# Kernel optimization log

Hardware: AMD Instinct MI355X
Metric: run time of the kernel (lower is better)

The kernel has to match this reference:

```python
import jax, jax.numpy as jnp
import numpy as np
from math import sqrt

B, S, D, H = 2, 2048, 1024, 16
HD = D // H


def setup_inputs() -> dict:
    key = jax.random.key(0)
    ks = jax.random.split(key, 5)
    std = 0.02
    return {
        "tensor_in": jax.random.normal(ks[0], (B, S, D), dtype=jnp.float32),
        "attention_mask": jnp.zeros((1, 1, S, S), dtype=jnp.float32),
        "Wq": jax.random.normal(ks[1], (D, D), dtype=jnp.float32) * std,
        "Wk": jax.random.normal(ks[2], (D, D), dtype=jnp.float32) * std,
        "Wv": jax.random.normal(ks[3], (D, D), dtype=jnp.float32) * std,
        "Wo": jax.random.normal(ks[4], (D, D), dtype=jnp.float32) * std,
    }


def reference(tensor_in, attention_mask, Wq, Wk, Wv, Wo):
    # nn.Linear(dim, dim, bias=False): y = x @ W.T, W is [out, in]
    q = tensor_in @ Wq.T  # [B,S,D]
    k = tensor_in @ Wk.T
    v = tensor_in @ Wv.T
    # split heads -> [B,H,S,HD]
    q = q.reshape(B, S, H, HD).transpose(0, 2, 1, 3)
    k = k.reshape(B, S, H, HD).transpose(0, 2, 1, 3)
    v = v.reshape(B, S, H, HD).transpose(0, 2, 1, 3)
    # scores [B,H,S,S]; note: mask added BEFORE scaling, scale = sqrt(full dim)
    scores = jnp.einsum("bhqd,bhkd->bhqk", q, k) + attention_mask
    weights = jax.nn.softmax(scores / sqrt(D), axis=-1)  # dropout = identity (eval)
    context = jnp.einsum("bhqk,bhkd->bhqd", weights, v)
    context = context.transpose(0, 2, 1, 3).reshape(B, S, D)
    return context @ Wo.T
```

## Files before the change

### kernel.cpp

```cpp
#include <hip/hip_runtime.h>

#define B_  2
#define S_  2048
#define D_  1024
#define H_  16
#define HD_ 64
#define M_  (B_*S_)

typedef __attribute__((ext_vector_type(8))) short  short8;
typedef __attribute__((ext_vector_type(4))) float  float4v;
typedef __attribute__((ext_vector_type(4))) int    int4v;
typedef __attribute__((ext_vector_type(4))) unsigned short ushort4v;

#define QSCALE 0.03125f

__device__ __forceinline__ unsigned short f_to_bf16bits(float f) {
    unsigned int x = __builtin_bit_cast(unsigned int, f);
    unsigned int lsb = (x >> 16) & 1u;
    x += 0x7fffu + lsb;
    return (unsigned short)(x >> 16);
}

__device__ __forceinline__ void async16(unsigned short* lds, const unsigned short* g) {
    __builtin_amdgcn_global_load_lds(
        (const __attribute__((address_space(1))) void*)g,
        (__attribute__((address_space(3))) void*)lds, 16, 0, 0);
}

__global__ __launch_bounds__(256) void cvt_bf16(
    const float* __restrict__ X,  const float* __restrict__ Wq,
    const float* __restrict__ Wk, const float* __restrict__ Wv,
    const float* __restrict__ Wo,
    unsigned short* __restrict__ Xb,  unsigned short* __restrict__ Wqb,
    unsigned short* __restrict__ Wkb, unsigned short* __restrict__ Wvb,
    unsigned short* __restrict__ Wob)
{
    const long t = (long)blockIdx.x * 256 + threadIdx.x;
    const long e = t * 8;
    const float* src; unsigned short* dst; long off;
    if      (e < 4194304) { src = X;  dst = Xb;  off = e; }
    else if (e < 5242880) { src = Wq; dst = Wqb; off = e - 4194304; }
    else if (e < 6291456) { src = Wk; dst = Wkb; off = e - 5242880; }
    else if (e < 7340032) { src = Wv; dst = Wvb; off = e - 6291456; }
    else                  { src = Wo; dst = Wob; off = e - 7340032; }
    float4v a = *(const float4v*)&src[off];
    float4v b = *(const float4v*)&src[off + 4];
    int4v o;
    o[0] = (int)f_to_bf16bits(a[0]) | ((int)f_to_bf16bits(a[1]) << 16);
    o[1] = (int)f_to_bf16bits(a[2]) | ((int)f_to_bf16bits(a[3]) << 16);
    o[2] = (int)f_to_bf16bits(b[0]) | ((int)f_to_bf16bits(b[1]) << 16);
    o[3] = (int)f_to_bf16bits(b[2]) | ((int)f_to_bf16bits(b[3]) << 16);
    *(int4v*)&dst[off] = o;
}

__global__ __launch_bounds__(256) void gemm_bt(
    const unsigned short* __restrict__ A,
    const unsigned short* __restrict__ B0,
    const unsigned short* __restrict__ B1,
    const unsigned short* __restrict__ B2,
    void* __restrict__ O0, void* __restrict__ O1, void* __restrict__ O2,
    int mode_base)
{
    const int K = 1024;
    const int z = blockIdx.z;
    const int mode = mode_base + z;
    const unsigned short* Aop;
    const unsigned short* Bop;
    void* Op = (z == 0) ? O0 : (z == 1) ? O1 : O2;
    int m0, n0;
    if (mode == 2) {
        Aop = B2; Bop = A;
        m0 = blockIdx.y * 128;
        n0 = blockIdx.x * 128;
    } else {
        Aop = A;
        Bop = (z == 0) ? B0 : (z == 1) ? B1 : B2;
        m0 = blockIdx.x * 128;
        n0 = blockIdx.y * 128;
    }

    __shared__ alignas(16) unsigned short As[128 * 64];
    __shared__ alignas(16) unsigned short Bs[128 * 64];

    const int tid  = threadIdx.x;
    const int wv   = tid >> 6;
    const int lane = tid & 63;
    const int wm   = wv >> 1, wn = wv & 1;
    const int q4   = lane >> 4, l15 = lane & 15;

    const unsigned short* gA[4];
    const unsigned short* gB[4];
    int slotj[4];
#pragma unroll
    for (int j = 0; j < 4; j++) {
        const int r = wv * 32 + j * 8 + (lane >> 3);
        const int c = (((lane & 7) ^ (r & 7)) * 8);
        gA[j] = Aop + (long)(m0 + r) * K + c;
        gB[j] = Bop + (long)(n0 + r) * K + c;
        slotj[j] = (wv * 32 + j * 8) * 64;
    }

    int aoff[2][4], boff[2][4];
#pragma unroll
    for (int ks = 0; ks < 2; ks++)
#pragma unroll
        for (int t = 0; t < 4; t++) {
            const int swz = (((ks * 4 + q4) ^ (l15 & 7)) * 8);
            aoff[ks][t] = (wm * 64 + t * 16 + l15) * 64 + swz;
            boff[ks][t] = (wn * 64 + t * 16 + l15) * 64 + swz;
        }

    float4v acc[4][4];
#pragma unroll
    for (int i = 0; i < 4; i++)
#pragma unroll
        for (int j = 0; j < 4; j++) acc[i][j] = (float4v)0.0f;

    for (int k0 = 0; k0 < K; k0 += 64) {
        __syncthreads();
#pragma unroll
        for (int j = 0; j < 4; j++) {
            async16(&As[slotj[j]], gA[j]);
            async16(&Bs[slotj[j]], gB[j]);
            gA[j] += 64; gB[j] += 64;
        }
        __syncthreads();

#pragma unroll
        for (int ks = 0; ks < 2; ks++) {
            short8 afr[4], bfr[4];
#pragma unroll
            for (int mt = 0; mt < 4; mt++) afr[mt] = *(const short8*)&As[aoff[ks][mt]];
#pragma unroll
            for (int nt = 0; nt < 4; nt++) bfr[nt] = *(const short8*)&Bs[boff[ks][nt]];
#pragma unroll
            for (int mt = 0; mt < 4; mt++)
#pragma unroll
                for (int nt = 0; nt < 4; nt++)
                    acc[mt][nt] = __builtin_amdgcn_mfma_f32_16x16x32_bf16(
                        afr[mt], bfr[nt], acc[mt][nt], 0, 0, 0);
        }
    }

#pragma unroll
    for (int mt = 0; mt < 4; mt++)
#pragma unroll
        for (int nt = 0; nt < 4; nt++)
#pragma unroll
            for (int r = 0; r < 4; r++) {
                const int m = m0 + wm * 64 + mt * 16 + q4 * 4 + r;
                const int n = n0 + wn * 64 + nt * 16 + l15;
                float v = acc[mt][nt][r];
                if (mode == 3) {
                    ((float*)Op)[(long)m * D_ + n] = v;
                } else if (mode == 2) {
                    const long off = (((long)(n >> 11) * H_ + (m >> 6)) * HD_ + (m & 63)) * S_ + (n & 2047);
                    ((unsigned short*)Op)[off] = f_to_bf16bits(v);
                } else {
                    const long off = ((long)((m >> 11) * H_ + (n >> 6)) * S_ + (m & 2047)) * HD_ + (n & 63);
                    if (mode == 0) v *= QSCALE;
                    ((unsigned short*)Op)[off] = f_to_bf16bits(v);
                }
            }
}

__global__ __launch_bounds__(256) void attn(
    const unsigned short* __restrict__ Q,
    const unsigned short* __restrict__ Kk,
    const unsigned short* __restrict__ Vt,
    const float* __restrict__ mask,
    unsigned short* __restrict__ ctx)
{
    __shared__ alignas(16) unsigned short Ks[64 * 64];
    __shared__ alignas(16) unsigned short Vs[64 * 64];
    __shared__ alignas(16) unsigned short Ps[4][16 * 64];

    const int tid  = threadIdx.x;
    const int wv   = tid >> 6;
    const int lane = tid & 63;
    const int q4   = lane >> 4, l15 = lane & 15;
    const int bh   = blockIdx.x;
    const int q0   = blockIdx.y * 64;

    const long head = (long)bh * S_ * HD_;

    const int qrow = q0 + wv * 16 + l15;
    short8 qfr[2];
    qfr[0] = *(const short8*)&Q[head + (long)qrow * HD_ + q4 * 8];
    qfr[1] = *(const short8*)&Q[head + (long)qrow * HD_ + 32 + q4 * 8];

    float l_acc[4];
#pragma unroll
    for (int r = 0; r < 4; r++) l_acc[r] = 0.0f;
    float4v oacc[4];
#pragma unroll
    for (int dt = 0; dt < 4; dt++) oacc[dt] = (float4v)0.0f;

    const int row0 = tid >> 3, row1 = row0 + 32, sch = tid & 7;
    const int cc   = ((sch ^ (row0 & 7)) * 8);
    const unsigned short* gK0 = Kk + head + (long)row0 * HD_ + cc;
    const unsigned short* gK1 = Kk + head + (long)row1 * HD_ + cc;
    const unsigned short* gV0 = Vt + head + (long)row0 * S_  + cc;
    const unsigned short* gV1 = Vt + head + (long)row1 * S_  + cc;
    const int ldsOff0 = row0 * 64 + sch * 8;
    const int ldsOff1 = row1 * 64 + sch * 8;

    const float* mrow[4];
#pragma unroll
    for (int r = 0; r < 4; r++)
        mrow[r] = mask + (long)(q0 + wv * 16 + q4 * 4 + r) * S_ + l15;

    int4v kr0 = *(const int4v*)gK0;
    int4v kr1 = *(const int4v*)gK1;
    int4v vr0 = *(const int4v*)gV0;
    int4v vr1 = *(const int4v*)gV1;
    float mv[4][4];
#pragma unroll
    for (int nt = 0; nt < 4; nt++)
#pragma unroll
        for (int r = 0; r < 4; r++) mv[nt][r] = mrow[r][nt * 16];

    const int pswz = (q4 & 1) * 4;
    const int psl3 = l15 >> 3;

    for (int k0 = 0; k0 < S_; k0 += 64) {
        __syncthreads();
        *(int4v*)&Ks[ldsOff0] = kr0;
        *(int4v*)&Ks[ldsOff1] = kr1;
        *(int4v*)&Vs[ldsOff0] = vr0;
        *(int4v*)&Vs[ldsOff1] = vr1;
        __syncthreads();

        if (k0 + 64 < S_) {
            kr0 = *(const int4v*)(gK0 + (long)(k0 + 64) * HD_);
            kr1 = *(const int4v*)(gK1 + (long)(k0 + 64) * HD_);
            vr0 = *(const int4v*)(gV0 + (k0 + 64));
            vr1 = *(const int4v*)(gV1 + (k0 + 64));
        }

        float4v sfr[4];
#pragma unroll
        for (int nt = 0; nt < 4; nt++) {
            const int row = nt * 16 + l15;
            const int p0 = ((q4       ^ (row & 7)) * 8);
            const int p1 = (((4 + q4) ^ (row & 7)) * 8);
            short8 kb0 = *(const short8*)&Ks[row * 64 + p0];
            short8 kb1 = *(const short8*)&Ks[row * 64 + p1];
            float4v s = (float4v)0.0f;
            s = __builtin_amdgcn_mfma_f32_16x16x32_bf16(qfr[0], kb0, s, 0, 0, 0);
            s = __builtin_amdgcn_mfma_f32_16x16x32_bf16(qfr[1], kb1, s, 0, 0, 0);
            sfr[nt] = s;
        }

        float mvn[4][4];
        const int knext = (k0 + 64 < S_) ? k0 + 64 : k0;
#pragma unroll
        for (int nt = 0; nt < 4; nt++)
#pragma unroll
            for (int r = 0; r < 4; r++) mvn[nt][r] = mrow[r][knext + nt * 16];

#pragma unroll
        for (int nt = 0; nt < 4; nt++)
#pragma unroll
            for (int r = 0; r < 4; r++) {
                const float p = __expf(fmaf(mv[nt][r], QSCALE, sfr[nt][r]));
                l_acc[r] += p;
                const int c8 = (nt * 2 + psl3) ^ (pswz + r);
                Ps[wv][(q4 * 4 + r) * 64 + c8 * 8 + (l15 & 7)] = f_to_bf16bits(p);
            }

        const int pp0 = ((q4       ^ (l15 & 7)) * 8);
        const int pp1 = (((4 + q4) ^ (l15 & 7)) * 8);
        short8 pf0 = *(const short8*)&Ps[wv][l15 * 64 + pp0];
        short8 pf1 = *(const short8*)&Ps[wv][l15 * 64 + pp1];

#pragma unroll
        for (int dt = 0; dt < 4; dt++) {
            const int row = dt * 16 + l15;
            const int p0 = ((q4       ^ (row & 7)) * 8);
            const int p1 = (((4 + q4) ^ (row & 7)) * 8);
            short8 vb0 = *(const short8*)&Vs[row * 64 + p0];
            short8 vb1 = *(const short8*)&Vs[row * 64 + p1];
            float4v o = oacc[dt];
            o = __builtin_amdgcn_mfma_f32_16x16x32_bf16(pf0, vb0, o, 0, 0, 0);
            o = __builtin_amdgcn_mfma_f32_16x16x32_bf16(pf1, vb1, o, 0, 0, 0);
            oacc[dt] = o;
        }

#pragma unroll
        for (int nt = 0; nt < 4; nt++)
#pragma unroll
            for (int r = 0; r < 4; r++) mv[nt][r] = mvn[nt][r];
    }

#pragma unroll
    for (int r = 0; r < 4; r++) {
#pragma unroll
        for (int off = 1; off < 16; off <<= 1)
            l_acc[r] += __shfl_xor(l_acc[r], off);
    }

    const int b = bh >> 4, h = bh & 15;
#pragma unroll
    for (int dt = 0; dt < 4; dt++)
#pragma unroll
        for (int r = 0; r < 4; r++) {
            const int qg = q0 + wv * 16 + q4 * 4 + r;
            const int d  = dt * 16 + l15;
            const float v = oacc[dt][r] / l_acc[r];
            ctx[((long)(b * S_ + qg)) * D_ + h * HD_ + d] = f_to_bf16bits(v);
        }
}

extern "C" void kernel_launch(void* const* d_in, const int* in_sizes, int n_in,
                              void* d_out, int out_size, void* d_ws, size_t ws_size,
                              hipStream_t stream) {
    const float* X    = (const float*)d_in[0];
    const float* mask = (const float*)d_in[1];
    const float* Wq   = (const float*)d_in[2];
    const float* Wk   = (const float*)d_in[3];
    const float* Wv   = (const float*)d_in[4];
    const float* Wo   = (const float*)d_in[5];
    float* out        = (float*)d_out;

    unsigned short* ws = (unsigned short*)d_ws;
    unsigned short* qws  = ws;
    unsigned short* kws  = ws + 4194304;
    unsigned short* vtws = ws + 8388608;
    unsigned short* ctx  = ws + 12582912;
    unsigned short* Xb   = ws + 16777216;
    unsigned short* Wqb  = ws + 20971520;
    unsigned short* Wkb  = ws + 22020096;
    unsigned short* Wvb  = ws + 23068672;
    unsigned short* Wob  = ws + 24117248;

    cvt_bf16<<<dim3(4096), 256, 0, stream>>>(X, Wq, Wk, Wv, Wo, Xb, Wqb, Wkb, Wvb, Wob);
    gemm_bt<<<dim3(32, 8, 3), 256, 0, stream>>>(Xb, Wqb, Wkb, Wvb, qws, kws, vtws, 0);
    attn<<<dim3(32, 32, 1), 256, 0, stream>>>(qws, kws, vtws, mask, ctx);
    gemm_bt<<<dim3(32, 8, 1), 256, 0, stream>>>(ctx, Wob, Wob, Wob, out, out, out, 3);
}
```

Baseline: 244.8 us.

## Register-prefetch GEMM tiles and shrink attention blocks to two waves

The GEMM drops direct global-to-LDS async loads in favour of register prefetch: the next K-tile is loaded into registers while the current tile is computed, then written to LDS after the barrier. The attention kernel moves from four waves covering 64 query rows to two waves covering 32 query rows, doubling the grid. Each thread now loads four K/V rows per tile so the 64-row staging still completes. The aim is to overlap global loads with MFMA work and to raise occupancy and block count in attention. The cost is more register pressure and K/V tiles fetched twice as often per query row.

```diff
diff --git a/kernel.cpp b/kernel.cpp
--- a/kernel.cpp
+++ b/kernel.cpp
@@ -19,12 +19,6 @@
     unsigned int lsb = (x >> 16) & 1u;
     x += 0x7fffu + lsb;
     return (unsigned short)(x >> 16);
-}
-
-__device__ __forceinline__ void async16(unsigned short* lds, const unsigned short* g) {
-    __builtin_amdgcn_global_load_lds(
-        (const __attribute__((address_space(1))) void*)g,
-        (__attribute__((address_space(3))) void*)lds, 16, 0, 0);
 }
 
 __global__ __launch_bounds__(256) void cvt_bf16(
@@ -90,14 +84,14 @@
 
     const unsigned short* gA[4];
     const unsigned short* gB[4];
-    int slotj[4];
+    int ldsoff[4];
 #pragma unroll
     for (int j = 0; j < 4; j++) {
         const int r = wv * 32 + j * 8 + (lane >> 3);
         const int c = (((lane & 7) ^ (r & 7)) * 8);
         gA[j] = Aop + (long)(m0 + r) * K + c;
         gB[j] = Bop + (long)(n0 + r) * K + c;
-        slotj[j] = (wv * 32 + j * 8) * 64;
+        ldsoff[j] = (wv * 32 + j * 8) * 64 + lane * 8;
     }
 
     int aoff[2][4], boff[2][4];
@@ -116,15 +110,31 @@
 #pragma unroll
         for (int j = 0; j < 4; j++) acc[i][j] = (float4v)0.0f;
 
+    int4v ar[4], br[4];
+#pragma unroll
+    for (int j = 0; j < 4; j++) {
+        ar[j] = *(const int4v*)gA[j];
+        br[j] = *(const int4v*)gB[j];
+        gA[j] += 64; gB[j] += 64;
+    }
+
     for (int k0 = 0; k0 < K; k0 += 64) {
         __syncthreads();
 #pragma unroll
         for (int j = 0; j < 4; j++) {
-            async16(&As[slotj[j]], gA[j]);
-            async16(&Bs[slotj[j]], gB[j]);
-            gA[j] += 64; gB[j] += 64;
+            *(int4v*)&As[ldsoff[j]] = ar[j];
+            *(int4v*)&Bs[ldsoff[j]] = br[j];
         }
         __syncthreads();
+
+        if (k0 + 64 < K) {
+#pragma unroll
+            for (int j = 0; j < 4; j++) {
+                ar[j] = *(const int4v*)gA[j];
+                br[j] = *(const int4v*)gB[j];
+                gA[j] += 64; gB[j] += 64;
+            }
+        }
 
 #pragma unroll
         for (int ks = 0; ks < 2; ks++) {
@@ -164,7 +174,7 @@
             }
 }
 
-__global__ __launch_bounds__(256) void attn(
+__global__ __launch_bounds__(128, 4) void attn(
     const unsigned short* __restrict__ Q,
     const unsigned short* __restrict__ Kk,
     const unsigned short* __restrict__ Vt,
@@ -173,14 +183,14 @@
 {
     __shared__ alignas(16) unsigned short Ks[64 * 64];
     __shared__ alignas(16) unsigned short Vs[64 * 64];
-    __shared__ alignas(16) unsigned short Ps[4][16 * 64];
+    __shared__ alignas(16) unsigned short Ps[2][16 * 64];
 
     const int tid  = threadIdx.x;
     const int wv   = tid >> 6;
     const int lane = tid & 63;
     const int q4   = lane >> 4, l15 = lane & 15;
     const int bh   = blockIdx.x;
-    const int q0   = blockIdx.y * 64;
+    const int q0   = blockIdx.y * 32;
 
     const long head = (long)bh * S_ * HD_;
 
@@ -196,24 +206,31 @@
 #pragma unroll
     for (int dt = 0; dt < 4; dt++) oacc[dt] = (float4v)0.0f;
 
-    const int row0 = tid >> 3, row1 = row0 + 32, sch = tid & 7;
-    const int cc   = ((sch ^ (row0 & 7)) * 8);
-    const unsigned short* gK0 = Kk + head + (long)row0 * HD_ + cc;
-    const unsigned short* gK1 = Kk + head + (long)row1 * HD_ + cc;
-    const unsigned short* gV0 = Vt + head + (long)row0 * S_  + cc;
-    const unsigned short* gV1 = Vt + head + (long)row1 * S_  + cc;
-    const int ldsOff0 = row0 * 64 + sch * 8;
-    const int ldsOff1 = row1 * 64 + sch * 8;
+    const int srow = tid >> 3;
+    const int sch  = tid & 7;
+    const int lc   = (sch ^ (srow & 7)) * 8;
+    const unsigned short* gK[4];
+    const unsigned short* gV[4];
+    int ldsOff[4];
+#pragma unroll
+    for (int j = 0; j < 4; j++) {
+        const int row = j * 16 + srow;
+        gK[j] = Kk + head + (long)row * HD_ + lc;
+        gV[j] = Vt + head + (long)row * S_  + lc;
+        ldsOff[j] = row * 64 + sch * 8;
+    }
 
     const float* mrow[4];
 #pragma unroll
     for (int r = 0; r < 4; r++)
         mrow[r] = mask + (long)(q0 + wv * 16 + q4 * 4 + r) * S_ + l15;
 
-    int4v kr0 = *(const int4v*)gK0;
-    int4v kr1 = *(const int4v*)gK1;
-    int4v vr0 = *(const int4v*)gV0;
-    int4v vr1 = *(const int4v*)gV1;
+    int4v kr[4], vr[4];
+#pragma unroll
+    for (int j = 0; j < 4; j++) {
+        kr[j] = *(const int4v*)gK[j];
+        vr[j] = *(const int4v*)gV[j];
+    }
     float mv[4][4];
 #pragma unroll
     for (int nt = 0; nt < 4; nt++)
@@ -225,17 +242,19 @@
 
     for (int k0 = 0; k0 < S_; k0 += 64) {
         __syncthreads();
-        *(int4v*)&Ks[ldsOff0] = kr0;
-        *(int4v*)&Ks[ldsOff1] = kr1;
-        *(int4v*)&Vs[ldsOff0] = vr0;
-        *(int4v*)&Vs[ldsOff1] = vr1;
+#pragma unroll
+        for (int j = 0; j < 4; j++) {
+            *(int4v*)&Ks[ldsOff[j]] = kr[j];
+            *(int4v*)&Vs[ldsOff[j]] = vr[j];
+        }
         __syncthreads();
 
         if (k0 + 64 < S_) {
-            kr0 = *(const int4v*)(gK0 + (long)(k0 + 64) * HD_);
-            kr1 = *(const int4v*)(gK1 + (long)(k0 + 64) * HD_);
-            vr0 = *(const int4v*)(gV0 + (k0 + 64));
-            vr1 = *(const int4v*)(gV1 + (k0 + 64));
+#pragma unroll
+            for (int j = 0; j < 4; j++) {
+                kr[j] = *(const int4v*)(gK[j] + (long)(k0 + 64) * HD_);
+                vr[j] = *(const int4v*)(gV[j] + (k0 + 64));
+            }
         }
 
         float4v sfr[4];
@@ -336,6 +355,6 @@
 
     cvt_bf16<<<dim3(4096), 256, 0, stream>>>(X, Wq, Wk, Wv, Wo, Xb, Wqb, Wkb, Wvb, Wob);
     gemm_bt<<<dim3(32, 8, 3), 256, 0, stream>>>(Xb, Wqb, Wkb, Wvb, qws, kws, vtws, 0);
-    attn<<<dim3(32, 32, 1), 256, 0, stream>>>(qws, kws, vtws, mask, ctx);
+    attn<<<dim3(32, 64, 1), 128, 0, stream>>>(qws, kws, vtws, mask, ctx);
     gemm_bt<<<dim3(32, 8, 1), 256, 0, stream>>>(ctx, Wob, Wob, Wob, out, out, out, 3);
 }
```

Result: slower. 392.4 us (+60.3%).

## Register-prefetch GEMM tiles, drop attention prefetch, fold log2e into Q scale

Applied to the files above, without the earlier changes.

The GEMM kernel no longer uses direct global-to-LDS async loads. It now loads the next K tile into registers while computing the current one, then stores them to LDS. The attention kernel drops its register double-buffering of K/V and loads directly before each LDS store. Folding log2(e) into the Q scale lets softmax use a raw exp2 instruction instead of __expf. The changes trade GEMM latency hiding and register pressure against the attention kernel's load overlap.

```diff
diff --git a/kernel.cpp b/kernel.cpp
--- a/kernel.cpp
+++ b/kernel.cpp
@@ -12,7 +12,7 @@
 typedef __attribute__((ext_vector_type(4))) int    int4v;
 typedef __attribute__((ext_vector_type(4))) unsigned short ushort4v;
 
-#define QSCALE 0.03125f
+#define PSCALE 0.0450843341f
 
 __device__ __forceinline__ unsigned short f_to_bf16bits(float f) {
     unsigned int x = __builtin_bit_cast(unsigned int, f);
@@ -21,10 +21,12 @@
     return (unsigned short)(x >> 16);
 }
 
-__device__ __forceinline__ void async16(unsigned short* lds, const unsigned short* g) {
-    __builtin_amdgcn_global_load_lds(
-        (const __attribute__((address_space(1))) void*)g,
-        (__attribute__((address_space(3))) void*)lds, 16, 0, 0);
+__device__ __forceinline__ float fast_exp2(float x) {
+#if __has_builtin(__builtin_amdgcn_exp2f)
+    return __builtin_amdgcn_exp2f(x);
+#else
+    return exp2f(x);
+#endif
 }
 
 __global__ __launch_bounds__(256) void cvt_bf16(
@@ -90,14 +92,14 @@
 
     const unsigned short* gA[4];
     const unsigned short* gB[4];
-    int slotj[4];
+    int ldsoff[4];
 #pragma unroll
     for (int j = 0; j < 4; j++) {
         const int r = wv * 32 + j * 8 + (lane >> 3);
         const int c = (((lane & 7) ^ (r & 7)) * 8);
         gA[j] = Aop + (long)(m0 + r) * K + c;
         gB[j] = Bop + (long)(n0 + r) * K + c;
-        slotj[j] = (wv * 32 + j * 8) * 64;
+        ldsoff[j] = (wv * 32 + j * 8) * 64 + lane * 8;
     }
 
     int aoff[2][4], boff[2][4];
@@ -116,15 +118,31 @@
 #pragma unroll
         for (int j = 0; j < 4; j++) acc[i][j] = (float4v)0.0f;
 
+    int4v ar[4], br[4];
+#pragma unroll
+    for (int j = 0; j < 4; j++) {
+        ar[j] = *(const int4v*)gA[j];
+        br[j] = *(const int4v*)gB[j];
+        gA[j] += 64; gB[j] += 64;
+    }
+
     for (int k0 = 0; k0 < K; k0 += 64) {
         __syncthreads();
 #pragma unroll
         for (int j = 0; j < 4; j++) {
-            async16(&As[slotj[j]], gA[j]);
-            async16(&Bs[slotj[j]], gB[j]);
-            gA[j] += 64; gB[j] += 64;
+            *(int4v*)&As[ldsoff[j]] = ar[j];
+            *(int4v*)&Bs[ldsoff[j]] = br[j];
         }
         __syncthreads();
+
+        if (k0 + 64 < K) {
+#pragma unroll
+            for (int j = 0; j < 4; j++) {
+                ar[j] = *(const int4v*)gA[j];
+                br[j] = *(const int4v*)gB[j];
+                gA[j] += 64; gB[j] += 64;
+            }
+        }
 
 #pragma unroll
         for (int ks = 0; ks < 2; ks++) {
@@ -158,7 +176,7 @@
                     ((unsigned short*)Op)[off] = f_to_bf16bits(v);
                 } else {
                     const long off = ((long)((m >> 11) * H_ + (n >> 6)) * S_ + (m & 2047)) * HD_ + (n & 63);
-                    if (mode == 0) v *= QSCALE;
+                    if (mode == 0) v *= PSCALE;
                     ((unsigned short*)Op)[off] = f_to_bf16bits(v);
                 }
             }
@@ -210,10 +228,6 @@
     for (int r = 0; r < 4; r++)
         mrow[r] = mask + (long)(q0 + wv * 16 + q4 * 4 + r) * S_ + l15;
 
-    int4v kr0 = *(const int4v*)gK0;
-    int4v kr1 = *(const int4v*)gK1;
-    int4v vr0 = *(const int4v*)gV0;
-    int4v vr1 = *(const int4v*)gV1;
     float mv[4][4];
 #pragma unroll
     for (int nt = 0; nt < 4; nt++)
@@ -225,18 +239,11 @@
 
     for (int k0 = 0; k0 < S_; k0 += 64) {
         __syncthreads();
-        *(int4v*)&Ks[ldsOff0] = kr0;
-        *(int4v*)&Ks[ldsOff1] = kr1;
-        *(int4v*)&Vs[ldsOff0] = vr0;
-        *(int4v*)&Vs[ldsOff1] = vr1;
+        *(int4v*)&Ks[ldsOff0] = *(const int4v*)(gK0 + (long)k0 * HD_);
+        *(int4v*)&Ks[ldsOff1] = *(const int4v*)(gK1 + (long)k0 * HD_);
+        *(int4v*)&Vs[ldsOff0] = *(const int4v*)(gV0 + k0);
+        *(int4v*)&Vs[ldsOff1] = *(const int4v*)(gV1 + k0);
         __syncthreads();
-
-        if (k0 + 64 < S_) {
-            kr0 = *(const int4v*)(gK0 + (long)(k0 + 64) * HD_);
-            kr1 = *(const int4v*)(gK1 + (long)(k0 + 64) * HD_);
-            vr0 = *(const int4v*)(gV0 + (k0 + 64));
-            vr1 = *(const int4v*)(gV1 + (k0 + 64));
-        }
 
         float4v sfr[4];
 #pragma unroll
@@ -263,7 +270,7 @@
         for (int nt = 0; nt < 4; nt++)
 #pragma unroll
             for (int r = 0; r < 4; r++) {
-                const float p = __expf(fmaf(mv[nt][r], QSCALE, sfr[nt][r]));
+                const float p = fast_exp2(fmaf(mv[nt][r], PSCALE, sfr[nt][r]));
                 l_acc[r] += p;
                 const int c8 = (nt * 2 + psl3) ^ (pswz + r);
                 Ps[wv][(q4 * 4 + r) * 64 + c8 * 8 + (l15 & 7)] = f_to_bf16bits(p);
```

Result: faster. 235.9 us (-3.6%).
